# Kernel optimization log

Hardware: AMD Instinct MI355X
Metric: run time of the kernel (lower is better)

## Reference

```python
import jax, jax.numpy as jnp
import numpy as np

B, T, N, IN, H, K = 8, 10, 50, 6, 256, 4
E = N * (N - 1)


def setup_inputs() -> dict:
    key = jax.random.key(0)
    ks = jax.random.split(key, 22)
    p = lambda k, shape: jax.random.normal(k, shape, jnp.float32) * 0.05
    return {
        "inputs": jax.random.normal(ks[0], (B, T, N, IN), jnp.float32),
        "sampled_edges": jax.random.uniform(ks[1], (B, T, E, K), dtype=jnp.float32),
        "msg_w1": p(ks[2], (K, H, 2 * H)), "msg_b1": p(ks[3], (K, H)),
        "msg_w2": p(ks[4], (K, H, H)), "msg_b2": p(ks[5], (K, H)),
        "w_hr": p(ks[6], (H, H)), "w_hi": p(ks[7], (H, H)), "w_hh": p(ks[8], (H, H)),
        "w_ir": p(ks[9], (H, IN)), "b_ir": p(ks[10], (H,)),
        "w_ii": p(ks[11], (H, IN)), "b_ii": p(ks[12], (H,)),
        "w_in": p(ks[13], (H, IN)), "b_in": p(ks[14], (H,)),
        "w_o1": p(ks[15], (H, H)), "b_o1": p(ks[16], (H,)),
        "w_o2": p(ks[17], (H, H)), "b_o2": p(ks[18], (H,)),
        "w_o3": p(ks[19], (IN, H)), "b_o3": p(ks[20], (IN,)),
    }


def reference(inputs, sampled_edges, msg_w1, msg_b1, msg_w2, msg_b2,
              w_hr, w_hi, w_hh, w_ir, b_ir, w_ii, b_ii, w_in, b_in,
              w_o1, b_o1, w_o2, b_o2, w_o3, b_o3):
    b, t, n, _ = inputs.shape
    k = msg_w1.shape[0]
    h = msg_w1.shape[1]
    # fully-connected directed graph, no self loops (static indices)
    send_np, recv_np = np.where(np.ones((n, n)) - np.eye(n))
    send = jnp.asarray(send_np)
    recv = jnp.asarray(recv_np)
    norm = float(k) - 1.0  # skip_first_edge_type = True

    def single_step(ins, rel, hidden):
        # ins: [B,N,IN], rel: [B,E,K], hidden: [B,N,H]
        pre = jnp.concatenate([hidden[:, recv], hidden[:, send]], axis=-1)  # [B,E,2H]
        all_msgs = jnp.zeros((b, pre.shape[1], h), inputs.dtype)
        for i in range(1, k):  # skip first edge type
            m = jnp.tanh(jnp.einsum('bef,hf->beh', pre, msg_w1[i]) + msg_b1[i])
            m = jnp.tanh(jnp.einsum('beh,jh->bej', m, msg_w2[i]) + msg_b2[i])
            all_msgs = all_msgs + m * rel[:, :, i:i + 1] / norm
        # scatter-add messages to receiver nodes (replaces onehot matmul)
        agg = jnp.zeros((b, n, h), inputs.dtype).at[:, recv].add(all_msgs) / (n - 1)
        r = jax.nn.sigmoid(ins @ w_ir.T + b_ir + agg @ w_hr.T)
        ig = jax.nn.sigmoid(ins @ w_ii.T + b_ii + agg @ w_hi.T)
        nn_ = jnp.tanh(ins @ w_in.T + b_in + r * (agg @ w_hh.T))
        hidden = (1 - ig) * nn_ + ig * hidden
        pred = jax.nn.relu(hidden @ w_o1.T + b_o1)
        pred = jax.nn.relu(pred @ w_o2.T + b_o2)
        pred = ins + (pred @ w_o3.T + b_o3)
        return pred, hidden

    x_t = jnp.swapaxes(inputs, 0, 1)         # [T,B,N,IN]
    e_t = jnp.swapaxes(sampled_edges, 0, 1)  # [T,B,E,K]
    h0 = jnp.zeros((b, n, h), inputs.dtype)

    def step(carry, xs):
        hidden, prev = carry
        xt, et, s = xs
        ins = jnp.where(s == 0, xt, prev)  # teacher_forcing=False: only step 0 uses inputs
        pred, hidden = single_step(ins, et, hidden)
        return (hidden, pred), pred

    _, preds = jax.lax.scan(step, (h0, jnp.zeros_like(x_t[0])), (x_t, e_t, jnp.arange(t)))
    return jnp.swapaxes(preds, 0, 1)  # [B,T,N,IN]
```

## Files before the change

### kernel.cpp

```cpp
#include <hip/hip_runtime.h>
#include <hip/hip_bf16.h>
#include <stdint.h>

#define B_ 8
#define T_ 10
#define N_ 50
#define IN_ 6
#define H_ 256
#define K_ 4
#define E_ 2450
#define ROWS 400
#define AP 102400

typedef __attribute__((ext_vector_type(8))) __bf16 bf16x8;
typedef __attribute__((ext_vector_type(4))) float f32x4;

__device__ __forceinline__ unsigned short f2bf(float x) {
    unsigned int u = __float_as_uint(x);
    u = (u + 0x7fffu + ((u >> 16) & 1u)) >> 16;
    return (unsigned short)u;
}
__device__ __forceinline__ unsigned pk2(float a, float b) {
    return (unsigned)f2bf(a) | ((unsigned)f2bf(b) << 16);
}
__device__ __forceinline__ float rcp_fast(float x) { return __builtin_amdgcn_rcpf(x); }
__device__ __forceinline__ float tanh_fast(float x) {
    float e = __expf(2.0f * x);
    return 1.0f - 2.0f * rcp_fast(e + 1.0f);
}
__device__ __forceinline__ float sigmoid_fast(float x) {
    return rcp_fast(1.0f + __expf(-x));
}

__global__ __launch_bounds__(256) void swizzle_weights(
        const float* __restrict__ w1, const float* __restrict__ w2,
        const float* __restrict__ whr, const float* __restrict__ whi,
        const float* __restrict__ whh, const float* __restrict__ wo1,
        const float* __restrict__ wo2,
        unsigned short* __restrict__ w1s, unsigned short* __restrict__ w2s,
        unsigned short* __restrict__ gws, unsigned short* __restrict__ wos,
        unsigned int* __restrict__ zero_region) {
    const int W1N = 3 * 16 * 16 * 64 * 8;
    const int W2N = 3 * 16 * 8 * 64 * 8;
    const int GWN = 3 * 65536;
    const int WON = 2 * 65536;
    int idx = blockIdx.x * 256 + threadIdx.x;
    if (idx < W1N) {
        int j = idx & 7, L = (idx >> 3) & 63, kt = (idx >> 9) & 15;
        int nt = (idx >> 13) & 15, i = idx >> 17;
        int n = nt * 16 + (L & 15);
        int k = kt * 32 + ((L >> 4) << 3) + j;
        w1s[idx] = f2bf(w1[((size_t)(i + 1) * H_ + n) * (2 * H_) + k]);
    } else if (idx < W1N + W2N) {
        int t = idx - W1N;
        int j = t & 7, L = (t >> 3) & 63, kt = (t >> 9) & 7;
        int nt = (t >> 12) & 15, i = t >> 16;
        int n = nt * 16 + (L & 15);
        int k = kt * 32 + ((L >> 4) << 3) + j;
        w2s[t] = f2bf(w2[((size_t)(i + 1) * H_ + n) * H_ + k]);
    } else if (idx < W1N + W2N + GWN) {
        int t = idx - (W1N + W2N);
        int j = t & 7, L = (t >> 3) & 63, kt = (t >> 9) & 7;
        int nt = (t >> 12) & 15, mat = t >> 16;
        int n = nt * 16 + (L & 15);
        int k = kt * 32 + ((L >> 4) << 3) + j;
        const float* src = (mat == 0) ? whr : (mat == 1) ? whi : whh;
        gws[t] = f2bf(src[(size_t)n * H_ + k]);
    } else if (idx < W1N + W2N + GWN + WON) {
        int t = idx - (W1N + W2N + GWN);
        int j = t & 7, L = (t >> 3) & 63, kt = (t >> 9) & 7;
        int nt = (t >> 12) & 15, g = t >> 16;
        int n = nt * 16 + (L & 15);
        int k = kt * 32 + ((L >> 4) << 3) + j;
        const float* src = (g == 0) ? wo1 : wo2;
        wos[t] = f2bf(src[(size_t)n * H_ + k]);
    } else {
        int t = idx - (W1N + W2N + GWN + WON);
        if (t < 153600) zero_region[t] = 0u;
    }
}

__global__ __launch_bounds__(256) void uv_kernel(
        const unsigned short* __restrict__ hb, const unsigned short* __restrict__ w1s,
        const float* __restrict__ b1, float* __restrict__ UV) {
    int mm = blockIdx.x / 6;
    int tyh = blockIdx.x % 6;
    int ty = tyh >> 1, half = tyh & 1;
    int lane = threadIdx.x & 63, wid = threadIdx.x >> 6;
    int col = lane & 15, q = lane >> 4;
    const bf16x8* w1f = (const bf16x8*)w1s;

    f32x4 acc[4];
    #pragma unroll
    for (int u = 0; u < 4; ++u) acc[u] = (f32x4){0.f, 0.f, 0.f, 0.f};
    #pragma unroll
    for (int kt = 0; kt < 8; ++kt) {
        bf16x8 a = *(const bf16x8*)&hb[(size_t)(mm * 16 + col) * H_ + kt * 32 + q * 8];
        #pragma unroll
        for (int u = 0; u < 4; ++u) {
            bf16x8 w = w1f[(size_t)((ty * 16 + wid * 4 + u) * 16 + half * 8 + kt) * 64 + lane];
            acc[u] = __builtin_amdgcn_mfma_f32_16x16x32_bf16(a, w, acc[u], 0, 0, 0);
        }
    }
    #pragma unroll
    for (int u = 0; u < 4; ++u) {
        float bias = (half == 0) ? b1[(ty + 1) * H_ + (wid * 4 + u) * 16 + col] : 0.0f;
        #pragma unroll
        for (int r = 0; r < 4; ++r)
            UV[((size_t)(mm * 16 + q * 4 + r) * 3 + ty) * 512 + half * 256 +
               (wid * 4 + u) * 16 + col] = acc[u][r] + bias;
    }
}

__global__ __launch_bounds__(256, 4) void msgagg_kernel(
        const float* __restrict__ UV, const float* __restrict__ edges,
        const unsigned short* __restrict__ w2s,
        const float* __restrict__ b2, float* __restrict__ aggP, int t) {
    __shared__ unsigned short m1F[32 * 512];
    __shared__ float relS[64];

    int ty = blockIdx.x / 400;
    int rem = blockIdx.x - ty * 400;
    int b = rem / 50;
    int r = rem - b * 50;
    int tid = threadIdx.x;
    int lane = tid & 63, wid = tid >> 6;
    int col = lane & 15, q = lane >> 4;

    if (tid < 64) {
        float v = 0.0f;
        if (tid < 50 && tid != r) {
            int e = tid * 49 + (r > tid ? r - 1 : r);
            v = edges[(((size_t)b * T_ + t) * E_ + e) * K_ + ty + 1];
        }
        relS[tid] = v;
    }

    {
        int row = wid * 16 + col;
        int sv = row < N_ ? row : N_ - 1;
        float fl = (row < N_) ? 1.0f : 0.0f;
        const float* Vrow = &UV[((size_t)(b * N_ + sv) * 3 + ty) * 512 + 256 + q * 8];
        const float* Urow = &UV[((size_t)(b * N_ + r) * 3 + ty) * 512 + q * 8];
        #pragma unroll
        for (int kt = 0; kt < 8; ++kt) {
            float4 v0 = *(const float4*)(Vrow + kt * 32);
            float4 v1 = *(const float4*)(Vrow + kt * 32 + 4);
            float4 u0 = *(const float4*)(Urow + kt * 32);
            float4 u1 = *(const float4*)(Urow + kt * 32 + 4);
            float m0 = tanh_fast(u0.x + v0.x) * fl;
            float m1 = tanh_fast(u0.y + v0.y) * fl;
            float m2 = tanh_fast(u0.z + v0.z) * fl;
            float m3 = tanh_fast(u0.w + v0.w) * fl;
            float m4 = tanh_fast(u1.x + v1.x) * fl;
            float m5 = tanh_fast(u1.y + v1.y) * fl;
            float m6 = tanh_fast(u1.z + v1.z) * fl;
            float m7 = tanh_fast(u1.w + v1.w) * fl;
            uint4 pk;
            pk.x = pk2(m0, m1); pk.y = pk2(m2, m3);
            pk.z = pk2(m4, m5); pk.w = pk2(m6, m7);
            *(uint4*)&m1F[(wid * 8 + kt) * 512 + lane * 8] = pk;
        }
    }
    __syncthreads();

    const bf16x8* w2f = (const bf16x8*)w2s;
    f32x4 acc[4][4];
    #pragma unroll
    for (int mt = 0; mt < 4; ++mt)
        #pragma unroll
        for (int u = 0; u < 4; ++u) acc[mt][u] = (f32x4){0.f, 0.f, 0.f, 0.f};

    #pragma unroll
    for (int kt = 0; kt < 8; ++kt) {
        bf16x8 a0 = *(const bf16x8*)&m1F[(0 * 8 + kt) * 512 + lane * 8];
        bf16x8 a1 = *(const bf16x8*)&m1F[(1 * 8 + kt) * 512 + lane * 8];
        bf16x8 a2 = *(const bf16x8*)&m1F[(2 * 8 + kt) * 512 + lane * 8];
        bf16x8 a3 = *(const bf16x8*)&m1F[(3 * 8 + kt) * 512 + lane * 8];
        #pragma unroll
        for (int u = 0; u < 4; ++u) {
            bf16x8 w = w2f[(size_t)((ty * 16 + wid * 4 + u) * 8 + kt) * 64 + lane];
            acc[0][u] = __builtin_amdgcn_mfma_f32_16x16x32_bf16(a0, w, acc[0][u], 0, 0, 0);
            acc[1][u] = __builtin_amdgcn_mfma_f32_16x16x32_bf16(a1, w, acc[1][u], 0, 0, 0);
            acc[2][u] = __builtin_amdgcn_mfma_f32_16x16x32_bf16(a2, w, acc[2][u], 0, 0, 0);
            acc[3][u] = __builtin_amdgcn_mfma_f32_16x16x32_bf16(a3, w, acc[3][u], 0, 0, 0);
        }
    }
    #pragma unroll
    for (int u = 0; u < 4; ++u) {
        float bias = b2[(ty + 1) * H_ + (wid * 4 + u) * 16 + col];
        float sum = 0.0f;
        #pragma unroll
        for (int mt = 0; mt < 4; ++mt)
            #pragma unroll
            for (int rg = 0; rg < 4; ++rg) {
                int row = mt * 16 + q * 4 + rg;
                sum += tanh_fast(acc[mt][u][rg] + bias) * relS[row];
            }
        sum += __shfl_xor(sum, 16);
        sum += __shfl_xor(sum, 32);
        if (lane < 16)
            aggP[(size_t)ty * AP + (size_t)(b * N_ + r) * H_ +
                 (wid * 4 + u) * 16 + col] = sum * (1.0f / 147.0f);
    }
}

__global__ __launch_bounds__(256) void node_kernel(
        const float* __restrict__ inputs, const float* __restrict__ aggP,
        const unsigned short* __restrict__ gws, const unsigned short* __restrict__ wos,
        float* __restrict__ hidden, unsigned short* __restrict__ hidden_bf,
        const float* __restrict__ w_ir, const float* __restrict__ b_ir,
        const float* __restrict__ w_ii, const float* __restrict__ b_ii,
        const float* __restrict__ w_in, const float* __restrict__ b_in,
        const float* __restrict__ b_o1, const float* __restrict__ b_o2,
        const float* __restrict__ w_o3, const float* __restrict__ b_o3,
        float* __restrict__ out, int t) {
    __shared__ unsigned short aggF[8 * 512];
    __shared__ unsigned short hnF[8 * 512];
    __shared__ unsigned short p1F[8 * 512];
    __shared__ float p2L[16 * 260];
    __shared__ float insS[16 * 6];

    int mm = blockIdx.x;
    int tid = threadIdx.x;
    int lane = tid & 63, wid = tid >> 6;
    int col = lane & 15, q = lane >> 4;

    const float* src = (t == 0) ? inputs : out;
    int tt = (t == 0) ? 0 : (t - 1);

    #pragma unroll
    for (int s = 0; s < 2; ++s) {
        int slot = tid + s * 256;
        int kt = slot >> 6, L = slot & 63;
        int row = mm * 16 + (L & 15);
        int k0 = kt * 32 + ((L >> 4) << 3);
        const float* p = &aggP[(size_t)row * H_ + k0];
        float4 a0 = *(const float4*)(p);
        float4 a1 = *(const float4*)(p + 4);
        float4 b0 = *(const float4*)(p + AP);
        float4 b1 = *(const float4*)(p + AP + 4);
        float4 c0 = *(const float4*)(p + 2 * AP);
        float4 c1 = *(const float4*)(p + 2 * AP + 4);
        uint4 pk;
        pk.x = pk2(a0.x + b0.x + c0.x, a0.y + b0.y + c0.y);
        pk.y = pk2(a0.z + b0.z + c0.z, a0.w + b0.w + c0.w);
        pk.z = pk2(a1.x + b1.x + c1.x, a1.y + b1.y + c1.y);
        pk.w = pk2(a1.z + b1.z + c1.z, a1.w + b1.w + c1.w);
        *(uint4*)&aggF[(size_t)kt * 512 + L * 8] = pk;
    }
    if (tid < 96) {
        int rl = tid / 6, c = tid - rl * 6;
        int row = mm * 16 + rl;
        int b = row / 50, n = row - b * 50;
        insS[rl * 6 + c] = src[(((size_t)b * T_ + tt) * N_ + n) * IN_ + c];
    }
    __syncthreads();

    const bf16x8* gwf = (const bf16x8*)gws;
    f32x4 acc[3][4];
    #pragma unroll
    for (int m = 0; m < 3; ++m)
        #pragma unroll
        for (int u = 0; u < 4; ++u) acc[m][u] = (f32x4){0.f, 0.f, 0.f, 0.f};
    #pragma unroll
    for (int kt = 0; kt < 8; ++kt) {
        bf16x8 a = *(const bf16x8*)&aggF[kt * 512 + lane * 8];
        #pragma unroll
        for (int m = 0; m < 3; ++m)
            #pragma unroll
            for (int u = 0; u < 4; ++u) {
                bf16x8 w = gwf[(size_t)((m * 16 + wid * 4 + u) * 8 + kt) * 64 + lane];
                acc[m][u] = __builtin_amdgcn_mfma_f32_16x16x32_bf16(a, w, acc[m][u], 0, 0, 0);
            }
    }

    #pragma unroll
    for (int u = 0; u < 4; ++u) {
        int h = (wid * 4 + u) * 16 + col;
        float bir = b_ir[h], bii = b_ii[h], bin_ = b_in[h];
        float wir[6], wii[6], win[6];
        #pragma unroll
        for (int c = 0; c < 6; ++c) {
            wir[c] = w_ir[h * 6 + c];
            wii[c] = w_ii[h * 6 + c];
            win[c] = w_in[h * 6 + c];
        }
        #pragma unroll
        for (int rg = 0; rg < 4; ++rg) {
            int rl = q * 4 + rg;
            int row = mm * 16 + rl;
            float xr = bir, xi = bii, xn = bin_;
            #pragma unroll
            for (int c = 0; c < 6; ++c) {
                float iv = insS[rl * 6 + c];
                xr += wir[c] * iv;
                xi += wii[c] * iv;
                xn += win[c] * iv;
            }
            float rgate = sigmoid_fast(xr + acc[0][u][rg]);
            float igate = sigmoid_fast(xi + acc[1][u][rg]);
            float nn = tanh_fast(xn + rgate * acc[2][u][rg]);
            size_t off = (size_t)row * H_ + h;
            float hold = hidden[off];
            float hnew = (1.0f - igate) * nn + igate * hold;
            hidden[off] = hnew;
            hidden_bf[off] = f2bf(hnew);
            hnF[(h >> 5) * 512 + (((h >> 3) & 3) * 16 + rl) * 8 + (h & 7)] = f2bf(hnew);
        }
    }
    __syncthreads();

    const bf16x8* wof = (const bf16x8*)wos;
    f32x4 a1v[4];
    #pragma unroll
    for (int u = 0; u < 4; ++u) a1v[u] = (f32x4){0.f, 0.f, 0.f, 0.f};
    #pragma unroll
    for (int kt = 0; kt < 8; ++kt) {
        bf16x8 a = *(const bf16x8*)&hnF[kt * 512 + lane * 8];
        #pragma unroll
        for (int u = 0; u < 4; ++u) {
            bf16x8 w = wof[(size_t)((wid * 4 + u) * 8 + kt) * 64 + lane];
            a1v[u] = __builtin_amdgcn_mfma_f32_16x16x32_bf16(a, w, a1v[u], 0, 0, 0);
        }
    }
    #pragma unroll
    for (int u = 0; u < 4; ++u) {
        int h = (wid * 4 + u) * 16 + col;
        float bo = b_o1[h];
        #pragma unroll
        for (int rg = 0; rg < 4; ++rg) {
            int rl = q * 4 + rg;
            float v = fmaxf(a1v[u][rg] + bo, 0.0f);
            p1F[(h >> 5) * 512 + (((h >> 3) & 3) * 16 + rl) * 8 + (h & 7)] = f2bf(v);
        }
    }
    __syncthreads();

    f32x4 a2v[4];
    #pragma unroll
    for (int u = 0; u < 4; ++u) a2v[u] = (f32x4){0.f, 0.f, 0.f, 0.f};
    #pragma unroll
    for (int kt = 0; kt < 8; ++kt) {
        bf16x8 a = *(const bf16x8*)&p1F[kt * 512 + lane * 8];
        #pragma unroll
        for (int u = 0; u < 4; ++u) {
            bf16x8 w = wof[(size_t)((16 + wid * 4 + u) * 8 + kt) * 64 + lane];
            a2v[u] = __builtin_amdgcn_mfma_f32_16x16x32_bf16(a, w, a2v[u], 0, 0, 0);
        }
    }
    #pragma unroll
    for (int u = 0; u < 4; ++u) {
        int h = (wid * 4 + u) * 16 + col;
        float bo = b_o2[h];
        #pragma unroll
        for (int rg = 0; rg < 4; ++rg) {
            int rl = q * 4 + rg;
            p2L[rl * 260 + h] = fmaxf(a2v[u][rg] + bo, 0.0f);
        }
    }
    __syncthreads();

    if (tid < 96) {
        int rl = tid / 6, c = tid - rl * 6;
        int row = mm * 16 + rl;
        float acc3 = b_o3[c];
        for (int k = 0; k < 256; k += 4) {
            float4 w = *(const float4*)&w_o3[c * 256 + k];
            float4 p = *(const float4*)&p2L[rl * 260 + k];
            acc3 += w.x * p.x + w.y * p.y + w.z * p.z + w.w * p.w;
        }
        int b = row / 50, n = row - b * 50;
        out[(((size_t)b * T_ + t) * N_ + n) * IN_ + c] = insS[rl * 6 + c] + acc3;
    }
}

extern "C" void kernel_launch(void* const* d_in, const int* in_sizes, int n_in,
                              void* d_out, int out_size, void* d_ws, size_t ws_size,
                              hipStream_t stream) {
    const float* inputs = (const float*)d_in[0];
    const float* edges  = (const float*)d_in[1];
    const float* msg_w1 = (const float*)d_in[2];
    const float* msg_b1 = (const float*)d_in[3];
    const float* msg_w2 = (const float*)d_in[4];
    const float* msg_b2 = (const float*)d_in[5];
    const float* w_hr = (const float*)d_in[6];
    const float* w_hi = (const float*)d_in[7];
    const float* w_hh = (const float*)d_in[8];
    const float* w_ir = (const float*)d_in[9];
    const float* b_ir = (const float*)d_in[10];
    const float* w_ii = (const float*)d_in[11];
    const float* b_ii = (const float*)d_in[12];
    const float* w_in = (const float*)d_in[13];
    const float* b_in = (const float*)d_in[14];
    const float* w_o1 = (const float*)d_in[15];
    const float* b_o1 = (const float*)d_in[16];
    const float* w_o2 = (const float*)d_in[17];
    const float* b_o2 = (const float*)d_in[18];
    const float* w_o3 = (const float*)d_in[19];
    const float* b_o3 = (const float*)d_in[20];
    float* out = (float*)d_out;

    char* ws = (char*)d_ws;
    float* hidden            = (float*)(ws);
    unsigned short* hidden_bf= (unsigned short*)(ws + 409600);
    float* UV                = (float*)(ws + 614400);
    float* aggP              = (float*)(ws + 3072000);
    unsigned short* w1s      = (unsigned short*)(ws + 4300800);
    unsigned short* w2s      = (unsigned short*)(ws + 5087232);
    unsigned short* gws      = (unsigned short*)(ws + 5480448);
    unsigned short* wos      = (unsigned short*)(ws + 5873664);

    swizzle_weights<<<dim3(4184), dim3(256), 0, stream>>>(
        msg_w1, msg_w2, w_hr, w_hi, w_hh, w_o1, w_o2, w1s, w2s, gws, wos,
        (unsigned int*)ws);

    for (int t = 0; t < T_; ++t) {
        uv_kernel<<<dim3(150), dim3(256), 0, stream>>>(hidden_bf, w1s, msg_b1, UV);
        msgagg_kernel<<<dim3(1200), dim3(256), 0, stream>>>(
            UV, edges, w2s, msg_b2, aggP, t);
        node_kernel<<<dim3(25), dim3(256), 0, stream>>>(
            inputs, aggP, gws, wos, hidden, hidden_bf,
            w_ir, b_ir, w_ii, b_ii, w_in, b_in, b_o1, b_o2, w_o3, b_o3, out, t);
    }
}
```

Baseline: 595.4 us.

## Fuse per-timestep kernels into one persistent kernel with software grid barriers

Replaces the 30 separate kernel launches (uv, msgagg, node per timestep) with a single persistent kernel of 256 blocks. An atomic-counter grid barrier separates the phases, and msgagg work units are strided across the blocks. This is meant to remove launch overhead and inter-kernel gaps. In exchange it adds spin-wait barrier cost, leaves most blocks idle during the uv and node phases, and relies on all 256 blocks being co-resident.

```diff
diff --git a/kernel.cpp b/kernel.cpp
--- a/kernel.cpp
+++ b/kernel.cpp
@@ -11,6 +11,7 @@
 #define E_ 2450
 #define ROWS 400
 #define AP 102400
+#define NBLK 256
 
 typedef __attribute__((ext_vector_type(8))) __bf16 bf16x8;
 typedef __attribute__((ext_vector_type(4))) float f32x4;
@@ -76,15 +77,28 @@
         wos[t] = f2bf(src[(size_t)n * H_ + k]);
     } else {
         int t = idx - (W1N + W2N + GWN + WON);
-        if (t < 153600) zero_region[t] = 0u;
-    }
-}
-
-__global__ __launch_bounds__(256) void uv_kernel(
-        const unsigned short* __restrict__ hb, const unsigned short* __restrict__ w1s,
-        const float* __restrict__ b1, float* __restrict__ UV) {
-    int mm = blockIdx.x / 6;
-    int tyh = blockIdx.x % 6;
+        if (t < 153664) zero_region[t] = 0u;
+    }
+}
+
+__device__ __forceinline__ void gridbar(unsigned* cnt, unsigned lg) {
+    __syncthreads();
+    if (threadIdx.x == 0) {
+        __threadfence();
+        atomicAdd(cnt, 1u);
+        unsigned target = (unsigned)NBLK * (lg + 1u);
+        while (atomicAdd(cnt, 0u) < target) __builtin_amdgcn_s_sleep(2);
+        __threadfence();
+    }
+    __syncthreads();
+}
+
+__device__ __forceinline__ void uv_body(
+        int unit, const unsigned short* __restrict__ hb,
+        const unsigned short* __restrict__ w1s, const float* __restrict__ b1,
+        float* __restrict__ UV) {
+    int mm = unit / 6;
+    int tyh = unit % 6;
     int ty = tyh >> 1, half = tyh & 1;
     int lane = threadIdx.x & 63, wid = threadIdx.x >> 6;
     int col = lane & 15, q = lane >> 4;
@@ -112,20 +126,19 @@
     }
 }
 
-__global__ __launch_bounds__(256, 4) void msgagg_kernel(
+__device__ __forceinline__ void msgagg_body(
+        int ty, int b, int r, char* smem,
         const float* __restrict__ UV, const float* __restrict__ edges,
-        const unsigned short* __restrict__ w2s,
-        const float* __restrict__ b2, float* __restrict__ aggP, int t) {
-    __shared__ unsigned short m1F[32 * 512];
-    __shared__ float relS[64];
-
-    int ty = blockIdx.x / 400;
-    int rem = blockIdx.x - ty * 400;
-    int b = rem / 50;
-    int r = rem - b * 50;
+        const unsigned short* __restrict__ w2s, const float* __restrict__ b2,
+        float* __restrict__ aggP, int t) {
+    unsigned short* m1F = (unsigned short*)smem;
+    float* relS = (float*)(smem + 32768);
+
     int tid = threadIdx.x;
     int lane = tid & 63, wid = tid >> 6;
     int col = lane & 15, q = lane >> 4;
+
+    __syncthreads();
 
     if (tid < 64) {
         float v = 0.0f;
@@ -135,7 +148,6 @@
         }
         relS[tid] = v;
     }
-
     {
         int row = wid * 16 + col;
         int sv = row < N_ ? row : N_ - 1;
@@ -205,7 +217,8 @@
     }
 }
 
-__global__ __launch_bounds__(256) void node_kernel(
+__device__ __forceinline__ void node_body(
+        int mm, char* smem,
         const float* __restrict__ inputs, const float* __restrict__ aggP,
         const unsigned short* __restrict__ gws, const unsigned short* __restrict__ wos,
         float* __restrict__ hidden, unsigned short* __restrict__ hidden_bf,
@@ -215,19 +228,20 @@
         const float* __restrict__ b_o1, const float* __restrict__ b_o2,
         const float* __restrict__ w_o3, const float* __restrict__ b_o3,
         float* __restrict__ out, int t) {
-    __shared__ unsigned short aggF[8 * 512];
-    __shared__ unsigned short hnF[8 * 512];
-    __shared__ unsigned short p1F[8 * 512];
-    __shared__ float p2L[16 * 260];
-    __shared__ float insS[16 * 6];
-
-    int mm = blockIdx.x;
+    unsigned short* aggF = (unsigned short*)smem;
+    unsigned short* hnF  = (unsigned short*)(smem + 8192);
+    unsigned short* p1F  = (unsigned short*)(smem + 16384);
+    float* p2L = (float*)(smem + 24576);
+    float* insS = (float*)(smem + 41216);
+
     int tid = threadIdx.x;
     int lane = tid & 63, wid = tid >> 6;
     int col = lane & 15, q = lane >> 4;
 
     const float* src = (t == 0) ? inputs : out;
     int tt = (t == 0) ? 0 : (t - 1);
+
+    __syncthreads();
 
     #pragma unroll
     for (int s = 0; s < 2; ++s) {
@@ -372,6 +386,48 @@
         }
         int b = row / 50, n = row - b * 50;
         out[(((size_t)b * T_ + t) * N_ + n) * IN_ + c] = insS[rl * 6 + c] + acc3;
+    }
+}
+
+__global__ __launch_bounds__(256) void step_kernel(
+        const float* __restrict__ inputs, const float* __restrict__ edges,
+        const float* __restrict__ msg_b1, const float* __restrict__ msg_b2,
+        const float* __restrict__ w_ir, const float* __restrict__ b_ir,
+        const float* __restrict__ w_ii, const float* __restrict__ b_ii,
+        const float* __restrict__ w_in, const float* __restrict__ b_in,
+        const float* __restrict__ b_o1, const float* __restrict__ b_o2,
+        const float* __restrict__ w_o3, const float* __restrict__ b_o3,
+        float* __restrict__ out, char* __restrict__ ws) {
+    __shared__ __align__(16) char smem[41600];
+
+    float* hidden             = (float*)(ws);
+    unsigned short* hidden_bf = (unsigned short*)(ws + 409600);
+    unsigned* barcnt          = (unsigned*)(ws + 614400);
+    float* UV                 = (float*)(ws + 614656);
+    float* aggP               = (float*)(ws + 3072256);
+    const unsigned short* w1s = (const unsigned short*)(ws + 4301056);
+    const unsigned short* w2s = (const unsigned short*)(ws + 5087488);
+    const unsigned short* gws = (const unsigned short*)(ws + 5480704);
+    const unsigned short* wos = (const unsigned short*)(ws + 5873920);
+
+    int bid = blockIdx.x;
+    unsigned bar = 0;
+
+    for (int t = 0; t < T_; ++t) {
+        if (bid < 150) uv_body(bid, hidden_bf, w1s, msg_b1, UV);
+        gridbar(barcnt, bar++);
+        for (int unit = bid; unit < 1200; unit += NBLK) {
+            int ty = unit / 400;
+            int rem = unit - ty * 400;
+            int b = rem / 50, r = rem - (rem / 50) * 50;
+            msgagg_body(ty, b, r, smem, UV, edges, w2s, msg_b2, aggP, t);
+        }
+        gridbar(barcnt, bar++);
+        if (bid < 25)
+            node_body(bid, smem, inputs, aggP, gws, wos, hidden, hidden_bf,
+                      w_ir, b_ir, w_ii, b_ii, w_in, b_in, b_o1, b_o2, w_o3, b_o3,
+                      out, t);
+        gridbar(barcnt, bar++);
     }
 }
 
@@ -400,27 +456,18 @@
     const float* w_o3 = (const float*)d_in[19];
     const float* b_o3 = (const float*)d_in[20];
     float* out = (float*)d_out;
-
-    char* ws = (char*)d_ws;
-    float* hidden            = (float*)(ws);
-    unsigned short* hidden_bf= (unsigned short*)(ws + 409600);
-    float* UV                = (float*)(ws + 614400);
-    float* aggP              = (float*)(ws + 3072000);
-    unsigned short* w1s      = (unsigned short*)(ws + 4300800);
-    unsigned short* w2s      = (unsigned short*)(ws + 5087232);
-    unsigned short* gws      = (unsigned short*)(ws + 5480448);
-    unsigned short* wos      = (unsigned short*)(ws + 5873664);
-
-    swizzle_weights<<<dim3(4184), dim3(256), 0, stream>>>(
+    char* wsp = (char*)d_ws;
+
+    unsigned short* w1s = (unsigned short*)(wsp + 4301056);
+    unsigned short* w2s = (unsigned short*)(wsp + 5087488);
+    unsigned short* gws = (unsigned short*)(wsp + 5480704);
+    unsigned short* wos = (unsigned short*)(wsp + 5873920);
+
+    swizzle_weights<<<dim3(4185), dim3(256), 0, stream>>>(
         msg_w1, msg_w2, w_hr, w_hi, w_hh, w_o1, w_o2, w1s, w2s, gws, wos,
-        (unsigned int*)ws);
-
-    for (int t = 0; t < T_; ++t) {
-        uv_kernel<<<dim3(150), dim3(256), 0, stream>>>(hidden_bf, w1s, msg_b1, UV);
-        msgagg_kernel<<<dim3(1200), dim3(256), 0, stream>>>(
-            UV, edges, w2s, msg_b2, aggP, t);
-        node_kernel<<<dim3(25), dim3(256), 0, stream>>>(
-            inputs, aggP, gws, wos, hidden, hidden_bf,
-            w_ir, b_ir, w_ii, b_ii, w_in, b_in, b_o1, b_o2, w_o3, b_o3, out, t);
-    }
-}
+        (unsigned int*)wsp);
+
+    step_kernel<<<dim3(NBLK), dim3(256), 0, stream>>>(
+        inputs, edges, msg_b1, msg_b2, w_ir, b_ir, w_ii, b_ii, w_in, b_in,
+        b_o1, b_o2, w_o3, b_o3, out, wsp);
+}
```

Measured after the change: 2.035 ms. +241.8%, slower.

## Fuse GRU node update into next step's UV projection kernel

Applied to the files above, without the earlier changes.

Removes the separate node kernel per timestep. Each of the 150 UV blocks now recomputes the node/GRU update for its 16-row tile of the previous step, then computes the message-layer-1 projection straight from the new hidden tile held in shared memory. A single final node kernel handles the last step. Hidden state is double-buffered so redundant blocks do not race with readers, and the bf16 hidden copy in global memory is dropped. This saves a launch and a global round trip per step, at the cost of doing the node computation six times over.

```diff
diff --git a/kernel.cpp b/kernel.cpp
--- a/kernel.cpp
+++ b/kernel.cpp
@@ -76,158 +76,28 @@
         wos[t] = f2bf(src[(size_t)n * H_ + k]);
     } else {
         int t = idx - (W1N + W2N + GWN + WON);
-        if (t < 153600) zero_region[t] = 0u;
-    }
-}
-
-__global__ __launch_bounds__(256) void uv_kernel(
-        const unsigned short* __restrict__ hb, const unsigned short* __restrict__ w1s,
-        const float* __restrict__ b1, float* __restrict__ UV) {
-    int mm = blockIdx.x / 6;
-    int tyh = blockIdx.x % 6;
-    int ty = tyh >> 1, half = tyh & 1;
-    int lane = threadIdx.x & 63, wid = threadIdx.x >> 6;
-    int col = lane & 15, q = lane >> 4;
-    const bf16x8* w1f = (const bf16x8*)w1s;
-
-    f32x4 acc[4];
-    #pragma unroll
-    for (int u = 0; u < 4; ++u) acc[u] = (f32x4){0.f, 0.f, 0.f, 0.f};
-    #pragma unroll
-    for (int kt = 0; kt < 8; ++kt) {
-        bf16x8 a = *(const bf16x8*)&hb[(size_t)(mm * 16 + col) * H_ + kt * 32 + q * 8];
-        #pragma unroll
-        for (int u = 0; u < 4; ++u) {
-            bf16x8 w = w1f[(size_t)((ty * 16 + wid * 4 + u) * 16 + half * 8 + kt) * 64 + lane];
-            acc[u] = __builtin_amdgcn_mfma_f32_16x16x32_bf16(a, w, acc[u], 0, 0, 0);
-        }
-    }
-    #pragma unroll
-    for (int u = 0; u < 4; ++u) {
-        float bias = (half == 0) ? b1[(ty + 1) * H_ + (wid * 4 + u) * 16 + col] : 0.0f;
-        #pragma unroll
-        for (int r = 0; r < 4; ++r)
-            UV[((size_t)(mm * 16 + q * 4 + r) * 3 + ty) * 512 + half * 256 +
-               (wid * 4 + u) * 16 + col] = acc[u][r] + bias;
-    }
-}
-
-__global__ __launch_bounds__(256, 4) void msgagg_kernel(
-        const float* __restrict__ UV, const float* __restrict__ edges,
-        const unsigned short* __restrict__ w2s,
-        const float* __restrict__ b2, float* __restrict__ aggP, int t) {
-    __shared__ unsigned short m1F[32 * 512];
-    __shared__ float relS[64];
-
-    int ty = blockIdx.x / 400;
-    int rem = blockIdx.x - ty * 400;
-    int b = rem / 50;
-    int r = rem - b * 50;
-    int tid = threadIdx.x;
-    int lane = tid & 63, wid = tid >> 6;
-    int col = lane & 15, q = lane >> 4;
-
-    if (tid < 64) {
-        float v = 0.0f;
-        if (tid < 50 && tid != r) {
-            int e = tid * 49 + (r > tid ? r - 1 : r);
-            v = edges[(((size_t)b * T_ + t) * E_ + e) * K_ + ty + 1];
-        }
-        relS[tid] = v;
-    }
-
-    {
-        int row = wid * 16 + col;
-        int sv = row < N_ ? row : N_ - 1;
-        float fl = (row < N_) ? 1.0f : 0.0f;
-        const float* Vrow = &UV[((size_t)(b * N_ + sv) * 3 + ty) * 512 + 256 + q * 8];
-        const float* Urow = &UV[((size_t)(b * N_ + r) * 3 + ty) * 512 + q * 8];
-        #pragma unroll
-        for (int kt = 0; kt < 8; ++kt) {
-            float4 v0 = *(const float4*)(Vrow + kt * 32);
-            float4 v1 = *(const float4*)(Vrow + kt * 32 + 4);
-            float4 u0 = *(const float4*)(Urow + kt * 32);
-            float4 u1 = *(const float4*)(Urow + kt * 32 + 4);
-            float m0 = tanh_fast(u0.x + v0.x) * fl;
-            float m1 = tanh_fast(u0.y + v0.y) * fl;
-            float m2 = tanh_fast(u0.z + v0.z) * fl;
-            float m3 = tanh_fast(u0.w + v0.w) * fl;
-            float m4 = tanh_fast(u1.x + v1.x) * fl;
-            float m5 = tanh_fast(u1.y + v1.y) * fl;
-            float m6 = tanh_fast(u1.z + v1.z) * fl;
-            float m7 = tanh_fast(u1.w + v1.w) * fl;
-            uint4 pk;
-            pk.x = pk2(m0, m1); pk.y = pk2(m2, m3);
-            pk.z = pk2(m4, m5); pk.w = pk2(m6, m7);
-            *(uint4*)&m1F[(wid * 8 + kt) * 512 + lane * 8] = pk;
-        }
-    }
-    __syncthreads();
-
-    const bf16x8* w2f = (const bf16x8*)w2s;
-    f32x4 acc[4][4];
-    #pragma unroll
-    for (int mt = 0; mt < 4; ++mt)
-        #pragma unroll
-        for (int u = 0; u < 4; ++u) acc[mt][u] = (f32x4){0.f, 0.f, 0.f, 0.f};
-
-    #pragma unroll
-    for (int kt = 0; kt < 8; ++kt) {
-        bf16x8 a0 = *(const bf16x8*)&m1F[(0 * 8 + kt) * 512 + lane * 8];
-        bf16x8 a1 = *(const bf16x8*)&m1F[(1 * 8 + kt) * 512 + lane * 8];
-        bf16x8 a2 = *(const bf16x8*)&m1F[(2 * 8 + kt) * 512 + lane * 8];
-        bf16x8 a3 = *(const bf16x8*)&m1F[(3 * 8 + kt) * 512 + lane * 8];
-        #pragma unroll
-        for (int u = 0; u < 4; ++u) {
-            bf16x8 w = w2f[(size_t)((ty * 16 + wid * 4 + u) * 8 + kt) * 64 + lane];
-            acc[0][u] = __builtin_amdgcn_mfma_f32_16x16x32_bf16(a0, w, acc[0][u], 0, 0, 0);
-            acc[1][u] = __builtin_amdgcn_mfma_f32_16x16x32_bf16(a1, w, acc[1][u], 0, 0, 0);
-            acc[2][u] = __builtin_amdgcn_mfma_f32_16x16x32_bf16(a2, w, acc[2][u], 0, 0, 0);
-            acc[3][u] = __builtin_amdgcn_mfma_f32_16x16x32_bf16(a3, w, acc[3][u], 0, 0, 0);
-        }
-    }
-    #pragma unroll
-    for (int u = 0; u < 4; ++u) {
-        float bias = b2[(ty + 1) * H_ + (wid * 4 + u) * 16 + col];
-        float sum = 0.0f;
-        #pragma unroll
-        for (int mt = 0; mt < 4; ++mt)
-            #pragma unroll
-            for (int rg = 0; rg < 4; ++rg) {
-                int row = mt * 16 + q * 4 + rg;
-                sum += tanh_fast(acc[mt][u][rg] + bias) * relS[row];
-            }
-        sum += __shfl_xor(sum, 16);
-        sum += __shfl_xor(sum, 32);
-        if (lane < 16)
-            aggP[(size_t)ty * AP + (size_t)(b * N_ + r) * H_ +
-                 (wid * 4 + u) * 16 + col] = sum * (1.0f / 147.0f);
-    }
-}
-
-__global__ __launch_bounds__(256) void node_kernel(
+        if (t < 102400) zero_region[t] = 0u;
+    }
+}
+
+__device__ __forceinline__ void node_part(
+        int mm, int tstep, unsigned short* aggF, unsigned short* hnF,
+        unsigned short* p1F, float* p2L, float* insS,
         const float* __restrict__ inputs, const float* __restrict__ aggP,
         const unsigned short* __restrict__ gws, const unsigned short* __restrict__ wos,
-        float* __restrict__ hidden, unsigned short* __restrict__ hidden_bf,
+        const float* __restrict__ hidden_old, float* __restrict__ hidden_new,
         const float* __restrict__ w_ir, const float* __restrict__ b_ir,
         const float* __restrict__ w_ii, const float* __restrict__ b_ii,
         const float* __restrict__ w_in, const float* __restrict__ b_in,
         const float* __restrict__ b_o1, const float* __restrict__ b_o2,
         const float* __restrict__ w_o3, const float* __restrict__ b_o3,
-        float* __restrict__ out, int t) {
-    __shared__ unsigned short aggF[8 * 512];
-    __shared__ unsigned short hnF[8 * 512];
-    __shared__ unsigned short p1F[8 * 512];
-    __shared__ float p2L[16 * 260];
-    __shared__ float insS[16 * 6];
-
-    int mm = blockIdx.x;
+        float* __restrict__ out) {
     int tid = threadIdx.x;
     int lane = tid & 63, wid = tid >> 6;
     int col = lane & 15, q = lane >> 4;
 
-    const float* src = (t == 0) ? inputs : out;
-    int tt = (t == 0) ? 0 : (t - 1);
+    const float* src = (tstep == 0) ? inputs : out;
+    int tt = (tstep == 0) ? 0 : (tstep - 1);
 
     #pragma unroll
     for (int s = 0; s < 2; ++s) {
@@ -302,10 +172,9 @@
             float igate = sigmoid_fast(xi + acc[1][u][rg]);
             float nn = tanh_fast(xn + rgate * acc[2][u][rg]);
             size_t off = (size_t)row * H_ + h;
-            float hold = hidden[off];
+            float hold = hidden_old[off];
             float hnew = (1.0f - igate) * nn + igate * hold;
-            hidden[off] = hnew;
-            hidden_bf[off] = f2bf(hnew);
+            hidden_new[off] = hnew;
             hnF[(h >> 5) * 512 + (((h >> 3) & 3) * 16 + rl) * 8 + (h & 7)] = f2bf(hnew);
         }
     }
@@ -371,7 +240,182 @@
             acc3 += w.x * p.x + w.y * p.y + w.z * p.z + w.w * p.w;
         }
         int b = row / 50, n = row - b * 50;
-        out[(((size_t)b * T_ + t) * N_ + n) * IN_ + c] = insS[rl * 6 + c] + acc3;
+        out[(((size_t)b * T_ + tstep) * N_ + n) * IN_ + c] = insS[rl * 6 + c] + acc3;
+    }
+}
+
+__global__ __launch_bounds__(256) void nodeuv_kernel(
+        const float* __restrict__ inputs, const float* __restrict__ aggP,
+        const unsigned short* __restrict__ gws, const unsigned short* __restrict__ wos,
+        const unsigned short* __restrict__ w1s, const float* __restrict__ msg_b1,
+        float* __restrict__ hbuf0, float* __restrict__ hbuf1,
+        const float* __restrict__ w_ir, const float* __restrict__ b_ir,
+        const float* __restrict__ w_ii, const float* __restrict__ b_ii,
+        const float* __restrict__ w_in, const float* __restrict__ b_in,
+        const float* __restrict__ b_o1, const float* __restrict__ b_o2,
+        const float* __restrict__ w_o3, const float* __restrict__ b_o3,
+        float* __restrict__ out, float* __restrict__ UV, int t) {
+    __shared__ unsigned short aggF[8 * 512];
+    __shared__ unsigned short hnF[8 * 512];
+    __shared__ unsigned short p1F[8 * 512];
+    __shared__ float p2L[16 * 260];
+    __shared__ float insS[16 * 6];
+
+    int mm = blockIdx.x / 6;
+    int tyh = blockIdx.x % 6;
+    int ty = tyh >> 1, half = tyh & 1;
+    int tid = threadIdx.x;
+    int lane = tid & 63, wid = tid >> 6;
+    int col = lane & 15, q = lane >> 4;
+
+    if (t > 0) {
+        const float* hold = ((t - 1) & 1) ? hbuf1 : hbuf0;
+        float* hnew = (t & 1) ? hbuf1 : hbuf0;
+        node_part(mm, t - 1, aggF, hnF, p1F, p2L, insS,
+                  inputs, aggP, gws, wos, hold, hnew,
+                  w_ir, b_ir, w_ii, b_ii, w_in, b_in, b_o1, b_o2, w_o3, b_o3, out);
+    } else {
+        #pragma unroll
+        for (int s = 0; s < 2; ++s)
+            *(uint4*)&hnF[(tid + s * 256) * 8] = make_uint4(0u, 0u, 0u, 0u);
+    }
+    __syncthreads();
+
+    const bf16x8* w1f = (const bf16x8*)w1s;
+    f32x4 acc[4];
+    #pragma unroll
+    for (int u = 0; u < 4; ++u) acc[u] = (f32x4){0.f, 0.f, 0.f, 0.f};
+    #pragma unroll
+    for (int kt = 0; kt < 8; ++kt) {
+        bf16x8 a = *(const bf16x8*)&hnF[kt * 512 + lane * 8];
+        #pragma unroll
+        for (int u = 0; u < 4; ++u) {
+            bf16x8 w = w1f[(size_t)((ty * 16 + wid * 4 + u) * 16 + half * 8 + kt) * 64 + lane];
+            acc[u] = __builtin_amdgcn_mfma_f32_16x16x32_bf16(a, w, acc[u], 0, 0, 0);
+        }
+    }
+    #pragma unroll
+    for (int u = 0; u < 4; ++u) {
+        float bias = (half == 0) ? msg_b1[(ty + 1) * H_ + (wid * 4 + u) * 16 + col] : 0.0f;
+        #pragma unroll
+        for (int r = 0; r < 4; ++r)
+            UV[((size_t)(mm * 16 + q * 4 + r) * 3 + ty) * 512 + half * 256 +
+               (wid * 4 + u) * 16 + col] = acc[u][r] + bias;
+    }
+}
+
+__global__ __launch_bounds__(256) void node_final_kernel(
+        const float* __restrict__ inputs, const float* __restrict__ aggP,
+        const unsigned short* __restrict__ gws, const unsigned short* __restrict__ wos,
+        float* __restrict__ hbuf0, float* __restrict__ hbuf1,
+        const float* __restrict__ w_ir, const float* __restrict__ b_ir,
+        const float* __restrict__ w_ii, const float* __restrict__ b_ii,
+        const float* __restrict__ w_in, const float* __restrict__ b_in,
+        const float* __restrict__ b_o1, const float* __restrict__ b_o2,
+        const float* __restrict__ w_o3, const float* __restrict__ b_o3,
+        float* __restrict__ out) {
+    __shared__ unsigned short aggF[8 * 512];
+    __shared__ unsigned short hnF[8 * 512];
+    __shared__ unsigned short p1F[8 * 512];
+    __shared__ float p2L[16 * 260];
+    __shared__ float insS[16 * 6];
+    const int t = T_ - 1;
+    const float* hold = ((t) & 1) ? hbuf1 : hbuf0;
+    float* hnew = ((t + 1) & 1) ? hbuf1 : hbuf0;
+    node_part(blockIdx.x, t, aggF, hnF, p1F, p2L, insS,
+              inputs, aggP, gws, wos, hold, hnew,
+              w_ir, b_ir, w_ii, b_ii, w_in, b_in, b_o1, b_o2, w_o3, b_o3, out);
+}
+
+__global__ __launch_bounds__(256, 4) void msgagg_kernel(
+        const float* __restrict__ UV, const float* __restrict__ edges,
+        const unsigned short* __restrict__ w2s,
+        const float* __restrict__ b2, float* __restrict__ aggP, int t) {
+    __shared__ unsigned short m1F[32 * 512];
+    __shared__ float relS[64];
+
+    int ty = blockIdx.x / 400;
+    int rem = blockIdx.x - ty * 400;
+    int b = rem / 50;
+    int r = rem - b * 50;
+    int tid = threadIdx.x;
+    int lane = tid & 63, wid = tid >> 6;
+    int col = lane & 15, q = lane >> 4;
+
+    if (tid < 64) {
+        float v = 0.0f;
+        if (tid < 50 && tid != r) {
+            int e = tid * 49 + (r > tid ? r - 1 : r);
+            v = edges[(((size_t)b * T_ + t) * E_ + e) * K_ + ty + 1];
+        }
+        relS[tid] = v;
+    }
+    {
+        int row = wid * 16 + col;
+        int sv = row < N_ ? row : N_ - 1;
+        float fl = (row < N_) ? 1.0f : 0.0f;
+        const float* Vrow = &UV[((size_t)(b * N_ + sv) * 3 + ty) * 512 + 256 + q * 8];
+        const float* Urow = &UV[((size_t)(b * N_ + r) * 3 + ty) * 512 + q * 8];
+        #pragma unroll
+        for (int kt = 0; kt < 8; ++kt) {
+            float4 v0 = *(const float4*)(Vrow + kt * 32);
+            float4 v1 = *(const float4*)(Vrow + kt * 32 + 4);
+            float4 u0 = *(const float4*)(Urow + kt * 32);
+            float4 u1 = *(const float4*)(Urow + kt * 32 + 4);
+            float m0 = tanh_fast(u0.x + v0.x) * fl;
+            float m1 = tanh_fast(u0.y + v0.y) * fl;
+            float m2 = tanh_fast(u0.z + v0.z) * fl;
+            float m3 = tanh_fast(u0.w + v0.w) * fl;
+            float m4 = tanh_fast(u1.x + v1.x) * fl;
+            float m5 = tanh_fast(u1.y + v1.y) * fl;
+            float m6 = tanh_fast(u1.z + v1.z) * fl;
+            float m7 = tanh_fast(u1.w + v1.w) * fl;
+            uint4 pk;
+            pk.x = pk2(m0, m1); pk.y = pk2(m2, m3);
+            pk.z = pk2(m4, m5); pk.w = pk2(m6, m7);
+            *(uint4*)&m1F[(wid * 8 + kt) * 512 + lane * 8] = pk;
+        }
+    }
+    __syncthreads();
+
+    const bf16x8* w2f = (const bf16x8*)w2s;
+    f32x4 acc[4][4];
+    #pragma unroll
+    for (int mt = 0; mt < 4; ++mt)
+        #pragma unroll
+        for (int u = 0; u < 4; ++u) acc[mt][u] = (f32x4){0.f, 0.f, 0.f, 0.f};
+
+    #pragma unroll
+    for (int kt = 0; kt < 8; ++kt) {
+        bf16x8 a0 = *(const bf16x8*)&m1F[(0 * 8 + kt) * 512 + lane * 8];
+        bf16x8 a1 = *(const bf16x8*)&m1F[(1 * 8 + kt) * 512 + lane * 8];
+        bf16x8 a2 = *(const bf16x8*)&m1F[(2 * 8 + kt) * 512 + lane * 8];
+        bf16x8 a3 = *(const bf16x8*)&m1F[(3 * 8 + kt) * 512 + lane * 8];
+        #pragma unroll
+        for (int u = 0; u < 4; ++u) {
+            bf16x8 w = w2f[(size_t)((ty * 16 + wid * 4 + u) * 8 + kt) * 64 + lane];
+            acc[0][u] = __builtin_amdgcn_mfma_f32_16x16x32_bf16(a0, w, acc[0][u], 0, 0, 0);
+            acc[1][u] = __builtin_amdgcn_mfma_f32_16x16x32_bf16(a1, w, acc[1][u], 0, 0, 0);
+            acc[2][u] = __builtin_amdgcn_mfma_f32_16x16x32_bf16(a2, w, acc[2][u], 0, 0, 0);
+            acc[3][u] = __builtin_amdgcn_mfma_f32_16x16x32_bf16(a3, w, acc[3][u], 0, 0, 0);
+        }
+    }
+    #pragma unroll
+    for (int u = 0; u < 4; ++u) {
+        float bias = b2[(ty + 1) * H_ + (wid * 4 + u) * 16 + col];
+        float sum = 0.0f;
+        #pragma unroll
+        for (int mt = 0; mt < 4; ++mt)
+            #pragma unroll
+            for (int rg = 0; rg < 4; ++rg) {
+                int row = mt * 16 + q * 4 + rg;
+                sum += tanh_fast(acc[mt][u][rg] + bias) * relS[row];
+            }
+        sum += __shfl_xor(sum, 16);
+        sum += __shfl_xor(sum, 32);
+        if (lane < 16)
+            aggP[(size_t)ty * AP + (size_t)(b * N_ + r) * H_ +
+                 (wid * 4 + u) * 16 + col] = sum * (1.0f / 147.0f);
     }
 }
 
@@ -400,27 +444,30 @@
     const float* w_o3 = (const float*)d_in[19];
     const float* b_o3 = (const float*)d_in[20];
     float* out = (float*)d_out;
-
     char* ws = (char*)d_ws;
-    float* hidden            = (float*)(ws);
-    unsigned short* hidden_bf= (unsigned short*)(ws + 409600);
-    float* UV                = (float*)(ws + 614400);
-    float* aggP              = (float*)(ws + 3072000);
-    unsigned short* w1s      = (unsigned short*)(ws + 4300800);
-    unsigned short* w2s      = (unsigned short*)(ws + 5087232);
-    unsigned short* gws      = (unsigned short*)(ws + 5480448);
-    unsigned short* wos      = (unsigned short*)(ws + 5873664);
-
-    swizzle_weights<<<dim3(4184), dim3(256), 0, stream>>>(
+
+    float* hbuf0         = (float*)(ws);
+    float* hbuf1         = (float*)(ws + 409600);
+    float* UV            = (float*)(ws + 819200);
+    float* aggP          = (float*)(ws + 3276800);
+    unsigned short* w1s  = (unsigned short*)(ws + 4505600);
+    unsigned short* w2s  = (unsigned short*)(ws + 5292032);
+    unsigned short* gws  = (unsigned short*)(ws + 5685248);
+    unsigned short* wos  = (unsigned short*)(ws + 6078464);
+
+    swizzle_weights<<<dim3(3984), dim3(256), 0, stream>>>(
         msg_w1, msg_w2, w_hr, w_hi, w_hh, w_o1, w_o2, w1s, w2s, gws, wos,
         (unsigned int*)ws);
 
     for (int t = 0; t < T_; ++t) {
-        uv_kernel<<<dim3(150), dim3(256), 0, stream>>>(hidden_bf, w1s, msg_b1, UV);
+        nodeuv_kernel<<<dim3(150), dim3(256), 0, stream>>>(
+            inputs, aggP, gws, wos, w1s, msg_b1, hbuf0, hbuf1,
+            w_ir, b_ir, w_ii, b_ii, w_in, b_in, b_o1, b_o2, w_o3, b_o3,
+            out, UV, t);
         msgagg_kernel<<<dim3(1200), dim3(256), 0, stream>>>(
             UV, edges, w2s, msg_b2, aggP, t);
-        node_kernel<<<dim3(25), dim3(256), 0, stream>>>(
-            inputs, aggP, gws, wos, hidden, hidden_bf,
-            w_ir, b_ir, w_ii, b_ii, w_in, b_in, b_o1, b_o2, w_o3, b_o3, out, t);
-    }
-}
+    }
+    node_final_kernel<<<dim3(25), dim3(256), 0, stream>>>(
+        inputs, aggP, gws, wos, hbuf0, hbuf1,
+        w_ir, b_ir, w_ii, b_ii, w_in, b_in, b_o1, b_o2, w_o3, b_o3, out);
+}
```

Measured after the change: 619.3 us. 4.0% more time.
